# Performance work log

Measured on AMD Instinct MI355X. Metric: run time of the kernel, lower is better.

The kernel has to match this reference:

```python
import jax, jax.numpy as jnp
import numpy as np

N = 2048      # atoms in one graph
C = 8         # energy_num_channels
CONV = 332.07156


def setup_inputs() -> dict:
    key = jax.random.key(0)
    ks = jax.random.split(key, 12)
    X = jax.random.normal(ks[0], (N, 3), dtype=jnp.float32) * 10.0   # coords (Angstrom-ish)
    embs = jax.random.normal(ks[1], (N, C), dtype=jnp.float32)        # GNN atom embeddings
    qs = jax.random.normal(ks[2], (N,), dtype=jnp.float32) * 0.5      # partial charges
    Ps = jnp.zeros((N, 3), dtype=jnp.float32)                          # dipoles (zeros, as in EnergyNet.forward)
    w0 = jax.random.uniform(ks[3], (N,), dtype=jnp.float32) * 0.5 + 0.1  # vdw_dep
    s0 = jax.random.uniform(ks[4], (N,), dtype=jnp.float32) + 1.0        # vdw_sig
    chainidx = jax.random.randint(ks[5], (N,), 0, 2)
    sf_elec = jax.random.normal(ks[6], (2 * C + 1, 1), dtype=jnp.float32) * 0.1
    sf_elec = sf_elec.at[-1, 0].set(1.0)
    born_factor = jax.random.normal(ks[7], (C,), dtype=jnp.float32) * 0.1 + 1.0
    die_factor = jax.random.normal(ks[8], (C,), dtype=jnp.float32) * 0.1 + 4.0
    depth_factor = jax.random.normal(ks[9], (2 * C, 1), dtype=jnp.float32) * 0.05 + 1.0
    radius_factor = jax.random.normal(ks[10], (2 * C, 1), dtype=jnp.float32) * 0.05 + 1.0
    return dict(X=X, embs=embs, qs=qs, Ps=Ps, w0=w0, s0=s0, chainidx=chainidx,
                sf_elec=sf_elec, born_factor=born_factor, die_factor=die_factor,
                depth_factor=depth_factor, radius_factor=radius_factor)


def _nan_guard(e):
    return jnp.where(jnp.isnan(e), jnp.asarray(1e-6, e.dtype), e)


def _energies(X, embs, qs, Ps, w0, s0, mask, sf_elec, born, die, depth, radius):
    # shared pairwise geometry (original recomputes this in each submodule)
    V = X[None, :, :] - X[:, None, :]               # V[i,j] = X[j]-X[i], [N,N,3]
    D = jnp.sqrt(jnp.sum(V * V + 1e-6, axis=-1))    # [N,N]
    Vp = V + 1e-6
    Vn = Vp / jnp.maximum(jnp.linalg.norm(Vp, axis=-1, keepdims=True), 1e-12)
    invD = 1.0 / (D + 1e-6)

    # ---- Electrostatics ----
    f = sf_elec[:, 0]
    # screening = emb_j . f[:C] + emb_i . f[C:2C] + invD * f[2C]  (decomposed matmul)
    sf = (embs @ f[:C])[None, :] + (embs @ f[C:2 * C])[:, None] + invD * f[2 * C]
    OqP = jnp.einsum('ijk,ik->ij', Vn, Ps)
    OPP = Ps @ Ps.T
    Q12 = jnp.outer(qs, qs)
    invD3 = invD * invD * invD
    E_qq = Q12 * invD * sf
    E_qP = OqP * invD * invD3
    E_PP = OPP * invD3 * invD3
    E_elec = 0.5 * jnp.sum(CONV * mask * (E_qq + E_qP + E_PP))
    E_elec = _nan_guard(E_elec)

    # ---- Solvation (calc_pair=False => only Born self term) ----
    atomic_die = embs @ die + 1e-6
    R = embs @ born + 1.0
    E_self = -(1.0 - 1.0 / atomic_die) * qs / (R + 1e-6)
    E_solv = CONV * jnp.sum(E_self) * 0.01
    E_solv = _nan_guard(E_solv)

    # ---- vdW ----
    rf = radius[:, 0]
    df = depth[:, 0]
    sig_r = jax.nn.sigmoid((embs @ rf[:C])[None, :] + (embs @ rf[C:])[:, None])
    # NB: original broadcasting makes s0_ij = 2*s0[j] (column-only), reproduced faithfully
    s = (2.0 * s0)[None, :] * (0.8 * sig_r + 0.4)
    repl = 5.0 * jnp.exp(-0.3 * D * D * D) * mask
    Dm = D - s
    attr = (jnp.exp(-(Dm - 0.3) ** 2) + jnp.exp(-3.0 * Dm * Dm)
            + jnp.exp(-10.0 * Dm * Dm)) / 3.0 * mask
    w0j = jnp.sqrt(w0 * w0 + 1e-6)[None, :]        # original w0_ij also column-only
    sig_d = jax.nn.sigmoid((embs @ df[:C])[None, :] + (embs @ df[C:])[:, None])
    w = w0j * (sig_d + 0.5)
    E_vdw = jnp.sum(-w * attr + repl)
    E_vdw = _nan_guard(E_vdw)

    return E_vdw, E_elec, E_solv


def reference(X, embs, qs, Ps, w0, s0, chainidx, sf_elec, born_factor, die_factor,
              depth_factor, radius_factor):
    mask = (chainidx[None, :] != chainidx[:, None]).astype(X.dtype)
    return _energies(X, embs, qs, Ps, w0, s0, mask,
                     sf_elec, born_factor, die_factor, depth_factor, radius_factor)
```

## Files before the change

kernel.cpp:

```cpp
#include <hip/hip_runtime.h>

#define NA 2048
#define CDIM 8
#define CONVF 332.07156f
#define TI 4
#define PAIR_GRID 516


__global__ __launch_bounds__(1024) void pre_kernel(
    const float* __restrict__ X,
    const float* __restrict__ embs,
    const float* __restrict__ qs,
    const float* __restrict__ Ps,
    const float* __restrict__ w0,
    const float* __restrict__ s0,
    const int* __restrict__ chain,
    const float* __restrict__ sf_elec,
    const float* __restrict__ born,
    const float* __restrict__ die,
    const float* __restrict__ depth,
    const float* __restrict__ radius,
    int* __restrict__ wsi,
    float4* __restrict__ g0, float4* __restrict__ g1,
    float4* __restrict__ g2, float4* __restrict__ g3,
    float* __restrict__ d_out)
{
    const int t = threadIdx.x;
    const int i0 = 2 * t, i1 = 2 * t + 1;

    float4 a0[2], a1[2], a2[2], a3[2];
    int flag[2];
    float es = 0.0f;

#pragma unroll
    for (int h = 0; h < 2; ++h) {
        const int i = (h == 0) ? i0 : i1;
        float e[CDIM];
#pragma unroll
        for (int k = 0; k < CDIM; ++k) e[k] = embs[i * CDIM + k];
        float sfA = 0.f, sfB = 0.f, rfA = 0.f, rfB = 0.f, dfA = 0.f, dfB = 0.f;
        float dieV = 0.f, Rv = 0.f;
#pragma unroll
        for (int k = 0; k < CDIM; ++k) {
            sfA  += e[k] * sf_elec[k];
            sfB  += e[k] * sf_elec[CDIM + k];
            rfA  += e[k] * radius[k];
            rfB  += e[k] * radius[CDIM + k];
            dfA  += e[k] * depth[k];
            dfB  += e[k] * depth[CDIM + k];
            dieV += e[k] * die[k];
            Rv   += e[k] * born[k];
        }
        dieV += 1e-6f;
        Rv += 1.0f;
        const float q = qs[i];
        es += -(1.0f - 1.0f / dieV) * q / (Rv + 1e-6f);

        const float erB = __expf(-rfB), edB = __expf(-dfB);
        const float erA = __expf(-rfA), edA = __expf(-dfA);
        const float w0j = sqrtf(w0[i] * w0[i] + 1e-6f);

        a0[h] = make_float4(X[i * 3 + 0], X[i * 3 + 1], X[i * 3 + 2], q);
        a1[h] = make_float4(sfA, erA, edA, w0j);
        a2[h] = make_float4(2.0f * s0[i], Ps[i * 3 + 0], Ps[i * 3 + 1], Ps[i * 3 + 2]);
        a3[h] = make_float4(sfB, erB, edB, 0.0f);
        flag[h] = (chain[i] == 0) ? 1 : 0;
    }

    const int lane = t & 63, wv = t >> 6;
    int cnt = flag[0] + flag[1];
    int x = cnt;
#pragma unroll
    for (int off = 1; off < 64; off <<= 1) {
        int y = __shfl_up(x, off);
        if (lane >= off) x += y;
    }
    const int excl = x - cnt;

    __shared__ int wsum[16];
    __shared__ float fsum[16];
    if (lane == 63) wsum[wv] = x;
    float esw = es;
#pragma unroll
    for (int off = 32; off > 0; off >>= 1) esw += __shfl_down(esw, off);
    if (lane == 0) fsum[wv] = esw;
    __syncthreads();

    int wbase = 0, tot = 0;
#pragma unroll
    for (int k = 0; k < 16; ++k) {
        int v = wsum[k];
        if (k < wv) wbase += v;
        tot += v;
    }
    const int base = wbase + excl;

    const int p0_0 = base;
    const int slot0 = flag[0] ? p0_0 : tot + (i0 - p0_0);
    const int p0_1 = base + flag[0];
    const int slot1 = flag[1] ? p0_1 : tot + (i1 - p0_1);

    g0[slot0] = a0[0]; g1[slot0] = a1[0]; g2[slot0] = a2[0]; g3[slot0] = a3[0];
    g0[slot1] = a0[1]; g1[slot1] = a1[1]; g2[slot1] = a2[1]; g3[slot1] = a3[1];

    if (t == 0) {
        float tt = 0.f;
#pragma unroll
        for (int k = 0; k < 16; ++k) tt += fsum[k];
        d_out[2] = CONVF * 0.01f * tt;
        d_out[0] = 0.0f;
        d_out[1] = 0.0f;
        wsi[0] = tot;
    }
}

__global__ __launch_bounds__(256) void pair_kernel(
    const int* __restrict__ cnt,
    const float4* __restrict__ g0, const float4* __restrict__ g1,
    const float4* __restrict__ g2, const float4* __restrict__ g3,
    const float* __restrict__ sf_elec,
    float* __restrict__ d_out)
{
    const int b = blockIdx.x, tid = threadIdx.x;
    const int n0 = cnt[0];
    const int B0 = (n0 + TI - 1) / TI;
    const int n1 = NA - n0;
    const int B1 = (n1 + TI - 1) / TI;
    if (b >= B0 + B1) return;

    int rbase, rend, jbeg, jend;
    if (b < B0) { rbase = b * TI;             rend = n0; jbeg = n0; jend = NA; }
    else        { rbase = n0 + (b - B0) * TI; rend = NA; jbeg = 0;  jend = n0; }

    const float f16 = sf_elec[2 * CDIM];

    float xi[TI], yi[TI], zi[TI], qi[TI], sfB[TI], erB[TI], edB[TI], val[TI];
    float psx[TI], psy[TI], psz[TI];
    bool hasPs = false;
#pragma unroll
    for (int t = 0; t < TI; ++t) {
        int r = rbase + t;
        val[t] = (r < rend) ? 1.0f : 0.0f;
        r = min(r, rend - 1);
        r = max(r, 0);
        float4 p0 = g0[r], p3 = g3[r], p2 = g2[r];
        xi[t] = p0.x; yi[t] = p0.y; zi[t] = p0.z; qi[t] = p0.w;
        sfB[t] = p3.x; erB[t] = p3.y; edB[t] = p3.z;
        psx[t] = p2.y; psy[t] = p2.z; psz[t] = p2.w;
        hasPs = hasPs || (psx[t] != 0.0f) || (psy[t] != 0.0f) || (psz[t] != 0.0f);
    }

    float acc_e[TI], acc_v[TI];
#pragma unroll
    for (int t = 0; t < TI; ++t) { acc_e[t] = 0.f; acc_v[t] = 0.f; }

    const float* g2f = (const float*)g2;

#pragma unroll 2
    for (int j = jbeg + tid; j < jend; j += 256) {
        const float4 a = g0[j];
        const float4 bb = g1[j];
        float s0x2, pjx = 0.f, pjy = 0.f, pjz = 0.f;
        if (hasPs) {
            float4 c2 = g2[j];
            s0x2 = c2.x; pjx = c2.y; pjy = c2.z; pjz = c2.w;
        } else {
            s0x2 = g2f[4 * j];
        }

#pragma unroll
        for (int t = 0; t < TI; ++t) {
            const float dx = a.x - xi[t], dy = a.y - yi[t], dz = a.z - zi[t];
            const float d2 = dx * dx + dy * dy + dz * dz + 3e-6f;
            const float D = sqrtf(d2);
            const float invD = __builtin_amdgcn_rcpf(D + 1e-6f);

            const float sf = bb.x + sfB[t] + invD * f16;
            float ee = qi[t] * a.w * invD * sf;
            if (hasPs) {
                const float vpx = dx + 1e-6f, vpy = dy + 1e-6f, vpz = dz + 1e-6f;
                float vn = sqrtf(vpx * vpx + vpy * vpy + vpz * vpz);
                vn = fmaxf(vn, 1e-12f);
                const float OqP = (vpx * psx[t] + vpy * psy[t] + vpz * psz[t]) *
                                  __builtin_amdgcn_rcpf(vn);
                const float OPP = psx[t] * pjx + psy[t] * pjy + psz[t] * pjz;
                const float invD2 = invD * invD;
                const float invD4 = invD2 * invD2;
                const float invD6 = invD4 * invD2;
                ee += OqP * invD4 + OPP * invD6;
            }
            acc_e[t] += ee;

            const float sig_r = __builtin_amdgcn_rcpf(fmaf(bb.y, erB[t], 1.0f));
            const float s = s0x2 * fmaf(0.8f, sig_r, 0.4f);
            const float Dm = D - s;
            const float Dm2 = Dm * Dm;
            const float t1 = __expf(-Dm2);
            const float ta = t1 * __expf(fmaf(0.6f, Dm, -0.09f));
            const float t2 = t1 * t1;
            const float t3 = t2 * t1;
            const float t4 = t2 * t2;
            const float t8 = t4 * t4;
            const float t10 = t8 * t2;
            const float attr = ta + t3 + t10;
            const float sig_d = __builtin_amdgcn_rcpf(fmaf(bb.z, edB[t], 1.0f));
            const float w = bb.w * (sig_d + 0.5f);
            const float repl = 5.0f * __expf(-0.3f * D * d2);
            acc_v[t] += repl - w * attr * (1.0f / 3.0f);
        }
    }

    float ae = 0.f, av = 0.f;
#pragma unroll
    for (int t = 0; t < TI; ++t) {
        ae += val[t] * acc_e[t];
        av += val[t] * acc_v[t];
    }
#pragma unroll
    for (int off = 32; off > 0; off >>= 1) {
        ae += __shfl_down(ae, off);
        av += __shfl_down(av, off);
    }
    __shared__ float se[4], sv[4];
    const int lane = tid & 63, wid = tid >> 6;
    if (lane == 0) { se[wid] = ae; sv[wid] = av; }
    __syncthreads();
    if (tid == 0) {
        atomicAdd(d_out + 1, 0.5f * CONVF * (se[0] + se[1] + se[2] + se[3]));
        atomicAdd(d_out + 0, sv[0] + sv[1] + sv[2] + sv[3]);
    }
}

extern "C" void kernel_launch(void* const* d_in, const int* in_sizes, int n_in,
                              void* d_out, int out_size, void* d_ws, size_t ws_size,
                              hipStream_t stream) {
    const float* X       = (const float*)d_in[0];
    const float* embs    = (const float*)d_in[1];
    const float* qs      = (const float*)d_in[2];
    const float* Ps      = (const float*)d_in[3];
    const float* w0      = (const float*)d_in[4];
    const float* s0      = (const float*)d_in[5];
    const int*   chain   = (const int*)d_in[6];
    const float* sf_elec = (const float*)d_in[7];
    const float* born    = (const float*)d_in[8];
    const float* die     = (const float*)d_in[9];
    const float* depth   = (const float*)d_in[10];
    const float* radius  = (const float*)d_in[11];
    float* out = (float*)d_out;

    int* wsi = (int*)d_ws;
    float4* g0 = (float4*)((char*)d_ws + 128);
    float4* g1 = g0 + NA;
    float4* g2 = g1 + NA;
    float4* g3 = g2 + NA;

    pre_kernel<<<1, 1024, 0, stream>>>(
        X, embs, qs, Ps, w0, s0, chain, sf_elec, born, die, depth, radius,
        wsi, g0, g1, g2, g3, out);
    pair_kernel<<<PAIR_GRID, 256, 0, stream>>>(wsi, g0, g1, g2, g3, sf_elec, out);
}
```

Measured before the change: 97.52 us.

## Parallelize preprocessing across blocks and stage j-chunks in LDS with larger row tiles

The preprocessing kernel moves from one 1024-thread block to nine 256-thread blocks. Each block recomputes the chain-0 prefix over all atoms, and a per-block partial solvation sum is reduced later by an extra pair-kernel block. The pair kernel now uses 512 threads and 8 rows per block, halving the grid. It cooperatively loads j-chunks of packed atom data into shared memory and splits the dipole and no-dipole paths into separate loops. This targets the serial single-block preprocessing and the global loads in the pair loop, at the cost of extra barriers, more registers per thread and fewer blocks to fill the GPU.

```diff
diff --git a/kernel.cpp b/kernel.cpp
--- a/kernel.cpp
+++ b/kernel.cpp
@@ -3,11 +3,13 @@
 #define NA 2048
 #define CDIM 8
 #define CONVF 332.07156f
-#define TI 4
-#define PAIR_GRID 516
-
-
-__global__ __launch_bounds__(1024) void pre_kernel(
+#define PTI 8
+#define PTHREADS 512
+#define CH 1024
+#define PAIR_GRID 258
+
+
+__global__ __launch_bounds__(256) void pre_kernel(
     const float* __restrict__ X,
     const float* __restrict__ embs,
     const float* __restrict__ qs,
@@ -21,198 +23,243 @@
     const float* __restrict__ depth,
     const float* __restrict__ radius,
     int* __restrict__ wsi,
+    float* __restrict__ wsf,
     float4* __restrict__ g0, float4* __restrict__ g1,
     float4* __restrict__ g2, float4* __restrict__ g3,
     float* __restrict__ d_out)
 {
-    const int t = threadIdx.x;
-    const int i0 = 2 * t, i1 = 2 * t + 1;
-
-    float4 a0[2], a1[2], a2[2], a3[2];
-    int flag[2];
-    float es = 0.0f;
-
-#pragma unroll
-    for (int h = 0; h < 2; ++h) {
-        const int i = (h == 0) ? i0 : i1;
-        float e[CDIM];
-#pragma unroll
-        for (int k = 0; k < CDIM; ++k) e[k] = embs[i * CDIM + k];
-        float sfA = 0.f, sfB = 0.f, rfA = 0.f, rfB = 0.f, dfA = 0.f, dfB = 0.f;
-        float dieV = 0.f, Rv = 0.f;
-#pragma unroll
-        for (int k = 0; k < CDIM; ++k) {
-            sfA  += e[k] * sf_elec[k];
-            sfB  += e[k] * sf_elec[CDIM + k];
-            rfA  += e[k] * radius[k];
-            rfB  += e[k] * radius[CDIM + k];
-            dfA  += e[k] * depth[k];
-            dfB  += e[k] * depth[CDIM + k];
-            dieV += e[k] * die[k];
-            Rv   += e[k] * born[k];
-        }
-        dieV += 1e-6f;
-        Rv += 1.0f;
-        const float q = qs[i];
-        es += -(1.0f - 1.0f / dieV) * q / (Rv + 1e-6f);
-
-        const float erB = __expf(-rfB), edB = __expf(-dfB);
-        const float erA = __expf(-rfA), edA = __expf(-dfA);
-        const float w0j = sqrtf(w0[i] * w0[i] + 1e-6f);
-
-        a0[h] = make_float4(X[i * 3 + 0], X[i * 3 + 1], X[i * 3 + 2], q);
-        a1[h] = make_float4(sfA, erA, edA, w0j);
-        a2[h] = make_float4(2.0f * s0[i], Ps[i * 3 + 0], Ps[i * 3 + 1], Ps[i * 3 + 2]);
-        a3[h] = make_float4(sfB, erB, edB, 0.0f);
-        flag[h] = (chain[i] == 0) ? 1 : 0;
-    }
-
+    const int b = blockIdx.x, t = threadIdx.x;
+    if (b == 8) {
+        if (t < 2) d_out[t] = 0.0f;
+        return;
+    }
+    const int i = b * 256 + t;
+
+    const int4 f0 = ((const int4*)chain)[2 * t];
+    const int4 f1 = ((const int4*)chain)[2 * t + 1];
+    const int s = (f0.x == 0) + (f0.y == 0) + (f0.z == 0) + (f0.w == 0) +
+                  (f1.x == 0) + (f1.y == 0) + (f1.z == 0) + (f1.w == 0);
     const int lane = t & 63, wv = t >> 6;
-    int cnt = flag[0] + flag[1];
-    int x = cnt;
+    int x = s;
 #pragma unroll
     for (int off = 1; off < 64; off <<= 1) {
         int y = __shfl_up(x, off);
         if (lane >= off) x += y;
     }
-    const int excl = x - cnt;
-
-    __shared__ int wsum[16];
-    __shared__ float fsum[16];
-    if (lane == 63) wsum[wv] = x;
-    float esw = es;
-#pragma unroll
-    for (int off = 32; off > 0; off >>= 1) esw += __shfl_down(esw, off);
-    if (lane == 0) fsum[wv] = esw;
+    __shared__ int wtot[4];
+    __shared__ int gpre[256];
+    __shared__ float fsum[4];
+    if (lane == 63) wtot[wv] = x;
     __syncthreads();
-
     int wbase = 0, tot = 0;
 #pragma unroll
-    for (int k = 0; k < 16; ++k) {
-        int v = wsum[k];
+    for (int k = 0; k < 4; ++k) {
+        int v = wtot[k];
         if (k < wv) wbase += v;
         tot += v;
     }
-    const int base = wbase + excl;
-
-    const int p0_0 = base;
-    const int slot0 = flag[0] ? p0_0 : tot + (i0 - p0_0);
-    const int p0_1 = base + flag[0];
-    const int slot1 = flag[1] ? p0_1 : tot + (i1 - p0_1);
-
-    g0[slot0] = a0[0]; g1[slot0] = a1[0]; g2[slot0] = a2[0]; g3[slot0] = a3[0];
-    g0[slot1] = a0[1]; g1[slot1] = a1[1]; g2[slot1] = a2[1]; g3[slot1] = a3[1];
-
+    gpre[t] = wbase + x - s;
+    __syncthreads();
+
+    const int g = i >> 3;
+    int base = gpre[g];
+    for (int a = (g << 3); a < i; ++a) base += (chain[a] == 0);
+    const int flag = (chain[i] == 0);
+    const int slot = flag ? base : tot + (i - base);
+
+    float e[CDIM];
+#pragma unroll
+    for (int k = 0; k < CDIM; ++k) e[k] = embs[i * CDIM + k];
+    float sfA = 0.f, sfB = 0.f, rfA = 0.f, rfB = 0.f, dfA = 0.f, dfB = 0.f;
+    float dieV = 0.f, Rv = 0.f;
+#pragma unroll
+    for (int k = 0; k < CDIM; ++k) {
+        sfA  += e[k] * sf_elec[k];
+        sfB  += e[k] * sf_elec[CDIM + k];
+        rfA  += e[k] * radius[k];
+        rfB  += e[k] * radius[CDIM + k];
+        dfA  += e[k] * depth[k];
+        dfB  += e[k] * depth[CDIM + k];
+        dieV += e[k] * die[k];
+        Rv   += e[k] * born[k];
+    }
+    dieV += 1e-6f;
+    Rv += 1.0f;
+    const float q = qs[i];
+    float es = -(1.0f - 1.0f / dieV) * q / (Rv + 1e-6f);
+
+    const float erA = __expf(-rfA), edA = __expf(-dfA);
+    const float erB = __expf(-rfB), edB = __expf(-dfB);
+    const float w0j = sqrtf(w0[i] * w0[i] + 1e-6f);
+
+    g0[slot] = make_float4(X[i * 3 + 0], X[i * 3 + 1], X[i * 3 + 2], q);
+    g1[slot] = make_float4(sfA, erA, edA, w0j);
+    g2[slot] = make_float4(2.0f * s0[i], Ps[i * 3 + 0], Ps[i * 3 + 1], Ps[i * 3 + 2]);
+    g3[slot] = make_float4(sfB, erB, edB, 0.0f);
+
+#pragma unroll
+    for (int off = 32; off > 0; off >>= 1) es += __shfl_down(es, off);
+    if (lane == 0) fsum[wv] = es;
+    __syncthreads();
     if (t == 0) {
-        float tt = 0.f;
-#pragma unroll
-        for (int k = 0; k < 16; ++k) tt += fsum[k];
-        d_out[2] = CONVF * 0.01f * tt;
-        d_out[0] = 0.0f;
-        d_out[1] = 0.0f;
-        wsi[0] = tot;
+        wsf[b] = fsum[0] + fsum[1] + fsum[2] + fsum[3];
+        if (b == 0) wsi[0] = tot;
     }
 }
 
-__global__ __launch_bounds__(256) void pair_kernel(
+__global__ __launch_bounds__(512) void pair_kernel(
     const int* __restrict__ cnt,
     const float4* __restrict__ g0, const float4* __restrict__ g1,
     const float4* __restrict__ g2, const float4* __restrict__ g3,
     const float* __restrict__ sf_elec,
+    const float* __restrict__ wsf,
     float* __restrict__ d_out)
 {
     const int b = blockIdx.x, tid = threadIdx.x;
+
+    if (b == PAIR_GRID - 1) {
+        if (tid == 0) {
+            float tt = 0.f;
+#pragma unroll
+            for (int k = 0; k < 8; ++k) tt += wsf[k];
+            d_out[2] = CONVF * 0.01f * tt;
+        }
+        return;
+    }
+
     const int n0 = cnt[0];
-    const int B0 = (n0 + TI - 1) / TI;
+    const int B0 = (n0 + PTI - 1) / PTI;
     const int n1 = NA - n0;
-    const int B1 = (n1 + TI - 1) / TI;
+    const int B1 = (n1 + PTI - 1) / PTI;
     if (b >= B0 + B1) return;
 
     int rbase, rend, jbeg, jend;
-    if (b < B0) { rbase = b * TI;             rend = n0; jbeg = n0; jend = NA; }
-    else        { rbase = n0 + (b - B0) * TI; rend = NA; jbeg = 0;  jend = n0; }
+    if (b < B0) { rbase = b * PTI;             rend = n0; jbeg = n0; jend = NA; }
+    else        { rbase = n0 + (b - B0) * PTI; rend = NA; jbeg = 0;  jend = n0; }
 
     const float f16 = sf_elec[2 * CDIM];
 
-    float xi[TI], yi[TI], zi[TI], qi[TI], sfB[TI], erB[TI], edB[TI], val[TI];
-    float psx[TI], psy[TI], psz[TI];
+    __shared__ float4 sa[CH];
+    __shared__ float4 sb[CH];
+    __shared__ float  sc[CH];
+    __shared__ float4 sps[PTI];
+    __shared__ float se[8], sv[8];
+
+    float xi[PTI], yi[PTI], zi[PTI], qi[PTI], sfB[PTI], erB[PTI], edB[PTI], val[PTI];
     bool hasPs = false;
 #pragma unroll
-    for (int t = 0; t < TI; ++t) {
+    for (int t = 0; t < PTI; ++t) {
         int r = rbase + t;
         val[t] = (r < rend) ? 1.0f : 0.0f;
-        r = min(r, rend - 1);
-        r = max(r, 0);
-        float4 p0 = g0[r], p3 = g3[r], p2 = g2[r];
+        r = max(min(r, rend - 1), 0);
+        const float4 p0 = g0[r], p3 = g3[r], p2 = g2[r];
         xi[t] = p0.x; yi[t] = p0.y; zi[t] = p0.z; qi[t] = p0.w;
         sfB[t] = p3.x; erB[t] = p3.y; edB[t] = p3.z;
-        psx[t] = p2.y; psy[t] = p2.z; psz[t] = p2.w;
-        hasPs = hasPs || (psx[t] != 0.0f) || (psy[t] != 0.0f) || (psz[t] != 0.0f);
-    }
-
-    float acc_e[TI], acc_v[TI];
-#pragma unroll
-    for (int t = 0; t < TI; ++t) { acc_e[t] = 0.f; acc_v[t] = 0.f; }
+        hasPs = hasPs || (p2.y != 0.0f) || (p2.z != 0.0f) || (p2.w != 0.0f);
+        if (tid == 0) sps[t] = p2;
+    }
+
+    float acc_e[PTI], acc_v[PTI];
+#pragma unroll
+    for (int t = 0; t < PTI; ++t) { acc_e[t] = 0.f; acc_v[t] = 0.f; }
 
     const float* g2f = (const float*)g2;
 
-#pragma unroll 2
-    for (int j = jbeg + tid; j < jend; j += 256) {
-        const float4 a = g0[j];
-        const float4 bb = g1[j];
-        float s0x2, pjx = 0.f, pjy = 0.f, pjz = 0.f;
-        if (hasPs) {
-            float4 c2 = g2[j];
-            s0x2 = c2.x; pjx = c2.y; pjy = c2.z; pjz = c2.w;
+    for (int jc = jbeg; jc < jend; jc += CH) {
+        const int nc = min(CH, jend - jc);
+        __syncthreads();
+        for (int k = tid; k < nc; k += PTHREADS) {
+            sa[k] = g0[jc + k];
+            sb[k] = g1[jc + k];
+            sc[k] = g2f[4 * (jc + k)];
+        }
+        __syncthreads();
+
+        if (!hasPs) {
+            for (int jo = tid; jo < nc; jo += PTHREADS) {
+                const float4 A = sa[jo];
+                const float4 B = sb[jo];
+                const float  S = sc[jo];
+#pragma unroll
+                for (int t = 0; t < PTI; ++t) {
+                    const float dx = A.x - xi[t], dy = A.y - yi[t], dz = A.z - zi[t];
+                    const float d2 = dx * dx + dy * dy + dz * dz + 3e-6f;
+                    const float D = sqrtf(d2);
+                    const float invD = __builtin_amdgcn_rcpf(D + 1e-6f);
+
+                    const float sf = B.x + sfB[t] + invD * f16;
+                    acc_e[t] += qi[t] * A.w * invD * sf;
+
+                    const float sig_r = __builtin_amdgcn_rcpf(fmaf(B.y, erB[t], 1.0f));
+                    const float s = S * fmaf(0.8f, sig_r, 0.4f);
+                    const float Dm = D - s;
+                    const float Dm2 = Dm * Dm;
+                    const float t1 = __expf(-Dm2);
+                    const float ta = t1 * __expf(fmaf(0.6f, Dm, -0.09f));
+                    const float t2 = t1 * t1;
+                    const float t3 = t2 * t1;
+                    const float t4 = t2 * t2;
+                    const float t8 = t4 * t4;
+                    const float t10 = t8 * t2;
+                    const float attr = ta + t3 + t10;
+                    const float sig_d = __builtin_amdgcn_rcpf(fmaf(B.z, edB[t], 1.0f));
+                    const float w = B.w * (sig_d + 0.5f);
+                    const float repl = 5.0f * __expf(-0.3f * D * d2);
+                    acc_v[t] += repl - w * attr * (1.0f / 3.0f);
+                }
+            }
         } else {
-            s0x2 = g2f[4 * j];
+            for (int jo = tid; jo < nc; jo += PTHREADS) {
+                const float4 A = sa[jo];
+                const float4 B = sb[jo];
+                const float  S = sc[jo];
+                const float4 Pj = g2[jc + jo];
+#pragma unroll
+                for (int t = 0; t < PTI; ++t) {
+                    const float dx = A.x - xi[t], dy = A.y - yi[t], dz = A.z - zi[t];
+                    const float d2 = dx * dx + dy * dy + dz * dz + 3e-6f;
+                    const float D = sqrtf(d2);
+                    const float invD = __builtin_amdgcn_rcpf(D + 1e-6f);
+
+                    const float sf = B.x + sfB[t] + invD * f16;
+                    float ee = qi[t] * A.w * invD * sf;
+                    const float4 Pi = sps[t];
+                    const float vpx = dx + 1e-6f, vpy = dy + 1e-6f, vpz = dz + 1e-6f;
+                    float vn = sqrtf(vpx * vpx + vpy * vpy + vpz * vpz);
+                    vn = fmaxf(vn, 1e-12f);
+                    const float OqP = (vpx * Pi.y + vpy * Pi.z + vpz * Pi.w) *
+                                      __builtin_amdgcn_rcpf(vn);
+                    const float OPP = Pi.y * Pj.y + Pi.z * Pj.z + Pi.w * Pj.w;
+                    const float invD2 = invD * invD;
+                    const float invD4 = invD2 * invD2;
+                    const float invD6 = invD4 * invD2;
+                    ee += OqP * invD4 + OPP * invD6;
+                    acc_e[t] += ee;
+
+                    const float sig_r = __builtin_amdgcn_rcpf(fmaf(B.y, erB[t], 1.0f));
+                    const float s = S * fmaf(0.8f, sig_r, 0.4f);
+                    const float Dm = D - s;
+                    const float Dm2 = Dm * Dm;
+                    const float t1 = __expf(-Dm2);
+                    const float ta = t1 * __expf(fmaf(0.6f, Dm, -0.09f));
+                    const float t2 = t1 * t1;
+                    const float t3 = t2 * t1;
+                    const float t4 = t2 * t2;
+                    const float t8 = t4 * t4;
+                    const float t10 = t8 * t2;
+                    const float attr = ta + t3 + t10;
+                    const float sig_d = __builtin_amdgcn_rcpf(fmaf(B.z, edB[t], 1.0f));
+                    const float w = B.w * (sig_d + 0.5f);
+                    const float repl = 5.0f * __expf(-0.3f * D * d2);
+                    acc_v[t] += repl - w * attr * (1.0f / 3.0f);
+                }
+            }
         }
-
-#pragma unroll
-        for (int t = 0; t < TI; ++t) {
-            const float dx = a.x - xi[t], dy = a.y - yi[t], dz = a.z - zi[t];
-            const float d2 = dx * dx + dy * dy + dz * dz + 3e-6f;
-            const float D = sqrtf(d2);
-            const float invD = __builtin_amdgcn_rcpf(D + 1e-6f);
-
-            const float sf = bb.x + sfB[t] + invD * f16;
-            float ee = qi[t] * a.w * invD * sf;
-            if (hasPs) {
-                const float vpx = dx + 1e-6f, vpy = dy + 1e-6f, vpz = dz + 1e-6f;
-                float vn = sqrtf(vpx * vpx + vpy * vpy + vpz * vpz);
-                vn = fmaxf(vn, 1e-12f);
-                const float OqP = (vpx * psx[t] + vpy * psy[t] + vpz * psz[t]) *
-                                  __builtin_amdgcn_rcpf(vn);
-                const float OPP = psx[t] * pjx + psy[t] * pjy + psz[t] * pjz;
-                const float invD2 = invD * invD;
-                const float invD4 = invD2 * invD2;
-                const float invD6 = invD4 * invD2;
-                ee += OqP * invD4 + OPP * invD6;
-            }
-            acc_e[t] += ee;
-
-            const float sig_r = __builtin_amdgcn_rcpf(fmaf(bb.y, erB[t], 1.0f));
-            const float s = s0x2 * fmaf(0.8f, sig_r, 0.4f);
-            const float Dm = D - s;
-            const float Dm2 = Dm * Dm;
-            const float t1 = __expf(-Dm2);
-            const float ta = t1 * __expf(fmaf(0.6f, Dm, -0.09f));
-            const float t2 = t1 * t1;
-            const float t3 = t2 * t1;
-            const float t4 = t2 * t2;
-            const float t8 = t4 * t4;
-            const float t10 = t8 * t2;
-            const float attr = ta + t3 + t10;
-            const float sig_d = __builtin_amdgcn_rcpf(fmaf(bb.z, edB[t], 1.0f));
-            const float w = bb.w * (sig_d + 0.5f);
-            const float repl = 5.0f * __expf(-0.3f * D * d2);
-            acc_v[t] += repl - w * attr * (1.0f / 3.0f);
-        }
     }
 
     float ae = 0.f, av = 0.f;
 #pragma unroll
-    for (int t = 0; t < TI; ++t) {
+    for (int t = 0; t < PTI; ++t) {
         ae += val[t] * acc_e[t];
         av += val[t] * acc_v[t];
     }
@@ -221,13 +268,15 @@
         ae += __shfl_down(ae, off);
         av += __shfl_down(av, off);
     }
-    __shared__ float se[4], sv[4];
     const int lane = tid & 63, wid = tid >> 6;
     if (lane == 0) { se[wid] = ae; sv[wid] = av; }
     __syncthreads();
     if (tid == 0) {
-        atomicAdd(d_out + 1, 0.5f * CONVF * (se[0] + se[1] + se[2] + se[3]));
-        atomicAdd(d_out + 0, sv[0] + sv[1] + sv[2] + sv[3]);
+        float te = 0.f, tv = 0.f;
+#pragma unroll
+        for (int k = 0; k < 8; ++k) { te += se[k]; tv += sv[k]; }
+        atomicAdd(d_out + 1, 0.5f * CONVF * te);
+        atomicAdd(d_out + 0, tv);
     }
 }
 
@@ -248,14 +297,16 @@
     const float* radius  = (const float*)d_in[11];
     float* out = (float*)d_out;
 
-    int* wsi = (int*)d_ws;
+    int*   wsi = (int*)d_ws;
+    float* wsf = (float*)((char*)d_ws + 64);
     float4* g0 = (float4*)((char*)d_ws + 128);
     float4* g1 = g0 + NA;
     float4* g2 = g1 + NA;
     float4* g3 = g2 + NA;
 
-    pre_kernel<<<1, 1024, 0, stream>>>(
+    pre_kernel<<<9, 256, 0, stream>>>(
         X, embs, qs, Ps, w0, s0, chain, sf_elec, born, die, depth, radius,
-        wsi, g0, g1, g2, g3, out);
-    pair_kernel<<<PAIR_GRID, 256, 0, stream>>>(wsi, g0, g1, g2, g3, sf_elec, out);
+        wsi, wsf, g0, g1, g2, g3, out);
+    pair_kernel<<<PAIR_GRID, PTHREADS, 0, stream>>>(
+        wsi, g0, g1, g2, g3, sf_elec, wsf, out);
 }
```

Result: faster. 93.11 us (-4.5%).
